# Kernel optimization log

Measured on AMD Instinct MI355X. Metric: run time of the kernel, lower is better.

## Reference

```python
import jax, jax.numpy as jnp
import numpy as np

N = 16384      # num_nodes
E = 524288     # num_edges (avg degree 32)
B = 32         # batch_size
D = 64         # input_dim
OUT = 64       # output_dim
K = 2          # max_diffusion_step
M = 2 * K + 1  # num_matrices = len(supports)*K + 1


def setup_inputs() -> dict:
    key = jax.random.key(0)
    k1, k2, k3, k4, k5 = jax.random.split(key, 5)
    inputs = jax.random.normal(k1, (B, N, D), dtype=jnp.float32)
    rows = jax.random.randint(k2, (E,), 0, N)
    cols = jax.random.randint(k3, (E,), 0, N)
    adj_vals = jax.random.uniform(k4, (E,), dtype=jnp.float32)
    # xavier_normal_ init for weights [D*M, OUT]
    std = (2.0 / (D * M + OUT)) ** 0.5
    weights = jax.random.normal(k5, (D * M, OUT), dtype=jnp.float32) * std
    biases = jnp.zeros((1, OUT), dtype=jnp.float32)  # bias_start = 0.0
    return dict(inputs=inputs, adj_vals=adj_vals, rows=rows, cols=cols,
                weights=weights, biases=biases)


def _spmm(vals, src, dst, x):
    # y[dst] += vals * x[src]; x: [N, F]  (sparse matrix-vector over edge list)
    return jax.ops.segment_sum(vals[:, None] * x[src], dst, num_segments=N)


def reference(inputs, adj_vals, rows, cols, weights, biases):
    b, n, d = inputs.shape
    # calculate_random_walk_matrix(A) = D_row^{-1} A ; support1 = its transpose
    # calculate_random_walk_matrix(A^T) = D_col^{-1} A^T ; support2 = its transpose
    drow = jax.ops.segment_sum(adj_vals, rows, num_segments=N)
    dcol = jax.ops.segment_sum(adj_vals, cols, num_segments=N)
    inv_drow = jnp.where(drow > 0, 1.0 / drow, 0.0)
    inv_dcol = jnp.where(dcol > 0, 1.0 / dcol, 0.0)
    vals1 = adj_vals * inv_drow[rows]  # support1 @ x: gather src=rows, scatter dst=cols
    vals2 = adj_vals * inv_dcol[cols]  # support2 @ x: gather src=cols, scatter dst=rows
    supports = [(vals1, rows, cols), (vals2, cols, rows)]

    # x0 layout: permute(1,2,0) -> [N, D, B] -> [N, D*B]
    x0 = jnp.transpose(inputs, (1, 2, 0)).reshape(n, d * b)
    xs = [x0]
    for vals, src, dst in supports:
        x1 = _spmm(vals, src, dst, x0)
        xs.append(x1)
        for _ in range(2, K + 1):
            x2 = 2.0 * _spmm(vals, src, dst, x1) - x0
            xs.append(x2)
            x1, x0 = x2, x1  # NOTE: x0 deliberately NOT reset between supports (matches torch src)
    x = jnp.stack(xs, axis=0).reshape(M, n, d, b)       # [M, N, D, B]
    x = jnp.transpose(x, (3, 1, 2, 0)).reshape(b * n, d * M)  # [B*N, D*M]
    out = x @ weights + biases
    return out.reshape(b, n, OUT)
```

## Files before the change

### kernel.cpp

```cpp
#include <hip/hip_runtime.h>
#include <stdint.h>

#define NN 16384
#define EE 524288
#define BB 32
#define DD 64
#define OO 64
#define MM 5
#define KK 320
#define KP 328

typedef __attribute__((ext_vector_type(8))) short short8;
typedef __attribute__((ext_vector_type(4))) float floatx4;

__device__ __forceinline__ float bf2f(unsigned short u) {
    return __uint_as_float(((unsigned int)u) << 16);
}
__device__ __forceinline__ unsigned short f2bf(float f) {
    unsigned int u = __float_as_uint(f);
    u += 0x7fffu + ((u >> 16) & 1u);
    return (unsigned short)(u >> 16);
}
__device__ __forceinline__ unsigned int pack2(float a, float b) {
    return (unsigned int)f2bf(a) | ((unsigned int)f2bf(b) << 16);
}

__global__ __launch_bounds__(256) void hist_kernel(
    const float* __restrict__ adj, const int* __restrict__ rows,
    const int* __restrict__ cols,
    float* __restrict__ drow, float* __restrict__ dcol,
    int* __restrict__ cnt_row, int* __restrict__ cnt_col)
{
    int e = blockIdx.x * 256 + threadIdx.x;
    if (e < EE) {
        float a = adj[e];
        int r = rows[e], c = cols[e];
        atomicAdd(&drow[r], a);
        atomicAdd(&dcol[c], a);
        atomicAdd(&cnt_row[r], 1);
        atomicAdd(&cnt_col[c], 1);
    }
}

__global__ __launch_bounds__(1024) void scan_kernel(
    const int* __restrict__ cnt_col, const int* __restrict__ cnt_row,
    int* __restrict__ off_col, int* __restrict__ off_row,
    int* __restrict__ cur_col, int* __restrict__ cur_row)
{
    const int* cnt = (blockIdx.x == 0) ? cnt_col : cnt_row;
    int* off = (blockIdx.x == 0) ? off_col : off_row;
    int* cur = (blockIdx.x == 0) ? cur_col : cur_row;

    __shared__ int part[1024];
    int t = threadIdx.x;
    int base = t * 16;
    int local[16];
    int s = 0;
#pragma unroll
    for (int i = 0; i < 16; i++) { local[i] = cnt[base + i]; s += local[i]; }
    part[t] = s;
    __syncthreads();
    for (int d = 1; d < 1024; d <<= 1) {
        int v = (t >= d) ? part[t - d] : 0;
        __syncthreads();
        part[t] += v;
        __syncthreads();
    }
    int run = (t == 0) ? 0 : part[t - 1];
#pragma unroll
    for (int i = 0; i < 16; i++) {
        off[base + i] = run;
        cur[base + i] = run;
        run += local[i];
    }
    if (t == 1023) off[NN] = run;
}

__global__ __launch_bounds__(256) void scatter_kernel(
    const float* __restrict__ adj, const int* __restrict__ rows,
    const int* __restrict__ cols,
    const float* __restrict__ drow, const float* __restrict__ dcol,
    int* __restrict__ cur_col, int* __restrict__ cur_row,
    int2* __restrict__ edge1, int2* __restrict__ edge2)
{
    int e = blockIdx.x * 256 + threadIdx.x;
    if (e < EE) {
        float a = adj[e];
        int r = rows[e], c = cols[e];
        float dr = drow[r];
        float idr = (dr > 0.f) ? (1.f / dr) : 0.f;
        float dc = dcol[c];
        float idc = (dc > 0.f) ? (1.f / dc) : 0.f;
        int p1 = atomicAdd(&cur_col[c], 1);
        edge1[p1] = make_int2(r, __float_as_int(a * idr));
        int p2 = atomicAdd(&cur_row[r], 1);
        edge2[p2] = make_int2(c, __float_as_int(a * idc));
    }
}

__global__ __launch_bounds__(256) void cast_kernel(
    const float* __restrict__ inp, unsigned short* __restrict__ x0)
{
    size_t i = ((size_t)blockIdx.x * 256 + threadIdx.x) * 8;
    float4 a = *(const float4*)(inp + i);
    float4 b = *(const float4*)(inp + i + 4);
    uint4 o;
    o.x = pack2(a.x, a.y);
    o.y = pack2(a.z, a.w);
    o.z = pack2(b.x, b.y);
    o.w = pack2(b.z, b.w);
    *(uint4*)(x0 + i) = o;
}

__global__ __launch_bounds__(256) void wprep_kernel(
    const float* __restrict__ W, unsigned short* __restrict__ Wt)
{
    int i = blockIdx.x * 256 + threadIdx.x;
    if (i < OO * KK) {
        int o = i / KK;
        int kp = i - o * KK;
        int m = kp >> 6;
        int d = kp & 63;
        Wt[i] = f2bf(W[(d * MM + m) * OO + o]);
    }
}

__global__ __launch_bounds__(256) void spmm_kernel(
    const unsigned short* __restrict__ xin,
    const unsigned short* __restrict__ z,
    unsigned short* __restrict__ xout,
    const int* __restrict__ off, const int2* __restrict__ edges,
    float alpha, float beta, int has_z)
{
    unsigned int l = blockIdx.x;
    int xcd  = l & 7;
    unsigned int s = l >> 3;
    int bhi  = s >> 9;
    int ntile = s & 511;
    int b = bhi * 8 + xcd;

    int t = threadIdx.x;
    int n = ntile * 32 + (t >> 3);
    unsigned int dgb = (unsigned int)(t & 7) * 16u;
    int e0 = off[n], e1 = off[n + 1];
    const char* xbB = (const char*)(xin + (size_t)b * NN * DD);

    float acc[8];
#pragma unroll
    for (int j = 0; j < 8; j++) acc[j] = 0.f;

#define FMA8(V, W)                                                        \
    do {                                                                  \
        acc[0] = fmaf((W), __uint_as_float((V).x << 16), acc[0]);         \
        acc[1] = fmaf((W), __uint_as_float((V).x & 0xffff0000u), acc[1]); \
        acc[2] = fmaf((W), __uint_as_float((V).y << 16), acc[2]);         \
        acc[3] = fmaf((W), __uint_as_float((V).y & 0xffff0000u), acc[3]); \
        acc[4] = fmaf((W), __uint_as_float((V).z << 16), acc[4]);         \
        acc[5] = fmaf((W), __uint_as_float((V).z & 0xffff0000u), acc[5]); \
        acc[6] = fmaf((W), __uint_as_float((V).w << 16), acc[6]);         \
        acc[7] = fmaf((W), __uint_as_float((V).w & 0xffff0000u), acc[7]); \
    } while (0)

    int ecnt = e1 - e0;
    int nb4 = ecnt >> 2;

    int2 ed0, ed1, ed2, ed3;
    if (nb4 > 0) {
        ed0 = edges[e0];
        ed1 = edges[e0 + 1];
        ed2 = edges[e0 + 2];
        ed3 = edges[e0 + 3];
    }
    for (int it = 0; it < nb4; ++it) {
        uint4 v0 = *(const uint4*)(xbB + (((unsigned int)ed0.x) << 7) + dgb);
        uint4 v1 = *(const uint4*)(xbB + (((unsigned int)ed1.x) << 7) + dgb);
        uint4 v2 = *(const uint4*)(xbB + (((unsigned int)ed2.x) << 7) + dgb);
        uint4 v3 = *(const uint4*)(xbB + (((unsigned int)ed3.x) << 7) + dgb);
        float w0 = __int_as_float(ed0.y);
        float w1 = __int_as_float(ed1.y);
        float w2 = __int_as_float(ed2.y);
        float w3 = __int_as_float(ed3.y);

        int2 nd0, nd1, nd2, nd3;
        int enext = e0 + (it + 1) * 4;
        if (it + 1 < nb4) {
            nd0 = edges[enext];
            nd1 = edges[enext + 1];
            nd2 = edges[enext + 2];
            nd3 = edges[enext + 3];
        }

        FMA8(v0, w0);
        FMA8(v1, w1);
        FMA8(v2, w2);
        FMA8(v3, w3);

        ed0 = nd0; ed1 = nd1; ed2 = nd2; ed3 = nd3;
    }
    for (int e = e0 + nb4 * 4; e < e1; ++e) {
        int2 ed = edges[e];
        float wv = __int_as_float(ed.y);
        uint4 v = *(const uint4*)(xbB + (((unsigned int)ed.x) << 7) + dgb);
        FMA8(v, wv);
    }
#undef FMA8

    size_t fo = ((size_t)b * NN + n) * DD + (dgb >> 1);
    if (has_z) {
        uint4 zv = *(const uint4*)(z + fo);
        float zf[8];
        zf[0] = __uint_as_float(zv.x << 16);
        zf[1] = __uint_as_float(zv.x & 0xffff0000u);
        zf[2] = __uint_as_float(zv.y << 16);
        zf[3] = __uint_as_float(zv.y & 0xffff0000u);
        zf[4] = __uint_as_float(zv.z << 16);
        zf[5] = __uint_as_float(zv.z & 0xffff0000u);
        zf[6] = __uint_as_float(zv.w << 16);
        zf[7] = __uint_as_float(zv.w & 0xffff0000u);
#pragma unroll
        for (int j = 0; j < 8; j++) acc[j] = alpha * acc[j] + beta * zf[j];
    }

    uint4 o;
    o.x = pack2(acc[0], acc[1]);
    o.y = pack2(acc[2], acc[3]);
    o.z = pack2(acc[4], acc[5]);
    o.w = pack2(acc[6], acc[7]);
    *(uint4*)(xout + fo) = o;
}

__global__ __launch_bounds__(256) void final_mfma(
    const unsigned short* __restrict__ X0, const unsigned short* __restrict__ X1,
    const unsigned short* __restrict__ X2, const unsigned short* __restrict__ X3,
    const unsigned short* __restrict__ X4,
    const unsigned short* __restrict__ Wt, const float* __restrict__ bias,
    float* __restrict__ out)
{
    __shared__ __align__(16) unsigned short A_lds[64 * KP];
    int blk = blockIdx.x;
    int b = blk >> 8;
    int n0 = (blk & 255) * 64;
    int t = threadIdx.x;
    const unsigned short* Xs[MM] = {X0, X1, X2, X3, X4};

#pragma unroll
    for (int i = 0; i < 10; i++) {
        int idx = t + i * 256;
        int dgv = (idx & 7) * 8;
        int row = (idx >> 3) & 63;
        int m = idx >> 9;
        uint4 v = *(const uint4*)(Xs[m] + ((size_t)b * NN + n0 + row) * DD + dgv);
        *(uint4*)&A_lds[row * KP + m * 64 + dgv] = v;
    }
    __syncthreads();

    int wave = t >> 6;
    int lane = t & 63;
    int col = lane & 15;
    int quad = lane >> 4;

    floatx4 acc[4];
#pragma unroll
    for (int ct = 0; ct < 4; ct++) acc[ct] = (floatx4){0.f, 0.f, 0.f, 0.f};

    const unsigned short* abase = &A_lds[(wave * 16 + col) * KP + quad * 8];
#pragma unroll
    for (int kt = 0; kt < 10; kt++) {
        short8 a = *(const short8*)(abase + kt * 32);
#pragma unroll
        for (int ct = 0; ct < 4; ct++) {
            short8 bf = *(const short8*)(Wt + (size_t)(ct * 16 + col) * KK + kt * 32 + quad * 8);
            acc[ct] = __builtin_amdgcn_mfma_f32_16x16x32_bf16(a, bf, acc[ct], 0, 0, 0);
        }
    }

    size_t rbase = (size_t)b * NN + n0 + wave * 16 + quad * 4;
#pragma unroll
    for (int ct = 0; ct < 4; ct++) {
        int o = ct * 16 + col;
        float bv = bias[o];
#pragma unroll
        for (int r = 0; r < 4; r++) {
            out[(rbase + r) * OO + o] = acc[ct][r] + bv;
        }
    }
}

extern "C" void kernel_launch(void* const* d_in, const int* in_sizes, int n_in,
                              void* d_out, int out_size, void* d_ws, size_t ws_size,
                              hipStream_t stream)
{
    (void)in_sizes; (void)n_in; (void)out_size; (void)ws_size;
    const float* inputs  = (const float*)d_in[0];
    const float* adj     = (const float*)d_in[1];
    const int*   rows    = (const int*)d_in[2];
    const int*   cols    = (const int*)d_in[3];
    const float* weights = (const float*)d_in[4];
    const float* bias    = (const float*)d_in[5];
    float* out = (float*)d_out;

    char* ws = (char*)d_ws;
    size_t off = 0;
    auto alloc = [&](size_t bytes) -> char* {
        char* p = ws + off;
        off = (off + bytes + 255) & ~(size_t)255;
        return p;
    };
    float* drow    = (float*)alloc(NN * 4);
    float* dcol    = (float*)alloc(NN * 4);
    int* cnt_col   = (int*)alloc(NN * 4);
    int* cnt_row   = (int*)alloc(NN * 4);
    int* off_col   = (int*)alloc((NN + 1) * 4);
    int* off_row   = (int*)alloc((NN + 1) * 4);
    int* cur_col   = (int*)alloc(NN * 4);
    int* cur_row   = (int*)alloc(NN * 4);
    int2* edge1    = (int2*)alloc((size_t)EE * 8);
    int2* edge2    = (int2*)alloc((size_t)EE * 8);
    unsigned short* Wt = (unsigned short*)alloc((size_t)OO * KK * 2);
    unsigned short* X[MM];
    for (int m = 0; m < MM; m++) X[m] = (unsigned short*)alloc((size_t)NN * BB * DD * 2);

    hipMemsetAsync(drow, 0, (size_t)NN * 4 * 4, stream);

    hist_kernel<<<EE / 256, 256, 0, stream>>>(adj, rows, cols, drow, dcol,
                                              cnt_row, cnt_col);
    scan_kernel<<<2, 1024, 0, stream>>>(cnt_col, cnt_row, off_col, off_row,
                                        cur_col, cur_row);
    scatter_kernel<<<EE / 256, 256, 0, stream>>>(adj, rows, cols, drow, dcol,
                                                 cur_col, cur_row, edge1, edge2);
    cast_kernel<<<(BB * NN * DD) / (256 * 8), 256, 0, stream>>>(inputs, X[0]);
    wprep_kernel<<<(OO * KK + 255) / 256, 256, 0, stream>>>(weights, Wt);

    const int SPMM_GRID = 512 * BB;

    spmm_kernel<<<SPMM_GRID, 256, 0, stream>>>(X[0], nullptr, X[1], off_col,
                                               edge1, 1.f, 0.f, 0);
    spmm_kernel<<<SPMM_GRID, 256, 0, stream>>>(X[1], X[0], X[2], off_col,
                                               edge1, 2.f, -1.f, 1);
    spmm_kernel<<<SPMM_GRID, 256, 0, stream>>>(X[1], nullptr, X[3], off_row,
                                               edge2, 1.f, 0.f, 0);
    spmm_kernel<<<SPMM_GRID, 256, 0, stream>>>(X[3], X[1], X[4], off_row,
                                               edge2, 2.f, -1.f, 1);

    final_mfma<<<BB * (NN / 64), 256, 0, stream>>>(X[0], X[1], X[2], X[3], X[4],
                                                   Wt, bias, out);
}
```

Baseline: 1.108 ms.

## Drop LDS staging in final GEMM and enlarge per-wave row tile to 64

The final dense projection kernel no longer stages the activation tile in shared memory. Each wave now loads its A fragments straight from global memory and computes a 64-row by 64-column output tile with 16 accumulators, so every weight fragment load is reused across four row tiles. Blocks cover 256 rows instead of 64, giving four times fewer blocks, and launch bounds request four blocks per SM. The aim is to remove the LDS round-trip and barrier and to cut redundant weight loads, at the cost of strided, less coalesced global loads for A and higher register pressure.

```diff
diff --git a/kernel.cpp b/kernel.cpp
--- a/kernel.cpp
+++ b/kernel.cpp
@@ -8,7 +8,6 @@
 #define OO 64
 #define MM 5
 #define KK 320
-#define KP 328
 
 typedef __attribute__((ext_vector_type(8))) short short8;
 typedef __attribute__((ext_vector_type(4))) float floatx4;
@@ -229,59 +228,83 @@
     *(uint4*)(xout + fo) = o;
 }
 
-__global__ __launch_bounds__(256) void final_mfma(
+__global__ __launch_bounds__(256, 4) void final_mfma(
     const unsigned short* __restrict__ X0, const unsigned short* __restrict__ X1,
     const unsigned short* __restrict__ X2, const unsigned short* __restrict__ X3,
     const unsigned short* __restrict__ X4,
     const unsigned short* __restrict__ Wt, const float* __restrict__ bias,
     float* __restrict__ out)
 {
-    __shared__ __align__(16) unsigned short A_lds[64 * KP];
     int blk = blockIdx.x;
-    int b = blk >> 8;
-    int n0 = (blk & 255) * 64;
+    int b = blk >> 6;
+    int n0 = (blk & 63) * 256;
     int t = threadIdx.x;
-    const unsigned short* Xs[MM] = {X0, X1, X2, X3, X4};
-
-#pragma unroll
-    for (int i = 0; i < 10; i++) {
-        int idx = t + i * 256;
-        int dgv = (idx & 7) * 8;
-        int row = (idx >> 3) & 63;
-        int m = idx >> 9;
-        uint4 v = *(const uint4*)(Xs[m] + ((size_t)b * NN + n0 + row) * DD + dgv);
-        *(uint4*)&A_lds[row * KP + m * 64 + dgv] = v;
-    }
-    __syncthreads();
-
     int wave = t >> 6;
     int lane = t & 63;
     int col = lane & 15;
     int quad = lane >> 4;
 
-    floatx4 acc[4];
-#pragma unroll
-    for (int ct = 0; ct < 4; ct++) acc[ct] = (floatx4){0.f, 0.f, 0.f, 0.f};
-
-    const unsigned short* abase = &A_lds[(wave * 16 + col) * KP + quad * 8];
-#pragma unroll
-    for (int kt = 0; kt < 10; kt++) {
-        short8 a = *(const short8*)(abase + kt * 32);
-#pragma unroll
-        for (int ct = 0; ct < 4; ct++) {
-            short8 bf = *(const short8*)(Wt + (size_t)(ct * 16 + col) * KK + kt * 32 + quad * 8);
-            acc[ct] = __builtin_amdgcn_mfma_f32_16x16x32_bf16(a, bf, acc[ct], 0, 0, 0);
-        }
-    }
-
-    size_t rbase = (size_t)b * NN + n0 + wave * 16 + quad * 4;
+    size_t rowbase = (size_t)b * NN + n0 + wave * 64;
+
+    floatx4 acc[4][4];
+#pragma unroll
+    for (int ct = 0; ct < 4; ct++)
+#pragma unroll
+        for (int rt = 0; rt < 4; rt++) acc[ct][rt] = (floatx4){0.f, 0.f, 0.f, 0.f};
+
+#define KSTEP(XP, m, h)                                                          \
+    {                                                                            \
+        const unsigned short* xa = (XP) + rowbase * DD + (h) * 32 + quad * 8;    \
+        short8 a0 = *(const short8*)(xa + (0 * 16 + col) * DD);                  \
+        short8 a1 = *(const short8*)(xa + (1 * 16 + col) * DD);                  \
+        short8 a2 = *(const short8*)(xa + (2 * 16 + col) * DD);                  \
+        short8 a3 = *(const short8*)(xa + (3 * 16 + col) * DD);                  \
+        const unsigned short* wb = Wt + ((m) * 2 + (h)) * 32 + quad * 8;         \
+        short8 b0 = *(const short8*)(wb + (0 * 16 + col) * KK);                  \
+        short8 b1 = *(const short8*)(wb + (1 * 16 + col) * KK);                  \
+        short8 b2 = *(const short8*)(wb + (2 * 16 + col) * KK);                  \
+        short8 b3 = *(const short8*)(wb + (3 * 16 + col) * KK);                  \
+        acc[0][0] = __builtin_amdgcn_mfma_f32_16x16x32_bf16(a0, b0, acc[0][0], 0, 0, 0); \
+        acc[0][1] = __builtin_amdgcn_mfma_f32_16x16x32_bf16(a1, b0, acc[0][1], 0, 0, 0); \
+        acc[0][2] = __builtin_amdgcn_mfma_f32_16x16x32_bf16(a2, b0, acc[0][2], 0, 0, 0); \
+        acc[0][3] = __builtin_amdgcn_mfma_f32_16x16x32_bf16(a3, b0, acc[0][3], 0, 0, 0); \
+        acc[1][0] = __builtin_amdgcn_mfma_f32_16x16x32_bf16(a0, b1, acc[1][0], 0, 0, 0); \
+        acc[1][1] = __builtin_amdgcn_mfma_f32_16x16x32_bf16(a1, b1, acc[1][1], 0, 0, 0); \
+        acc[1][2] = __builtin_amdgcn_mfma_f32_16x16x32_bf16(a2, b1, acc[1][2], 0, 0, 0); \
+        acc[1][3] = __builtin_amdgcn_mfma_f32_16x16x32_bf16(a3, b1, acc[1][3], 0, 0, 0); \
+        acc[2][0] = __builtin_amdgcn_mfma_f32_16x16x32_bf16(a0, b2, acc[2][0], 0, 0, 0); \
+        acc[2][1] = __builtin_amdgcn_mfma_f32_16x16x32_bf16(a1, b2, acc[2][1], 0, 0, 0); \
+        acc[2][2] = __builtin_amdgcn_mfma_f32_16x16x32_bf16(a2, b2, acc[2][2], 0, 0, 0); \
+        acc[2][3] = __builtin_amdgcn_mfma_f32_16x16x32_bf16(a3, b2, acc[2][3], 0, 0, 0); \
+        acc[3][0] = __builtin_amdgcn_mfma_f32_16x16x32_bf16(a0, b3, acc[3][0], 0, 0, 0); \
+        acc[3][1] = __builtin_amdgcn_mfma_f32_16x16x32_bf16(a1, b3, acc[3][1], 0, 0, 0); \
+        acc[3][2] = __builtin_amdgcn_mfma_f32_16x16x32_bf16(a2, b3, acc[3][2], 0, 0, 0); \
+        acc[3][3] = __builtin_amdgcn_mfma_f32_16x16x32_bf16(a3, b3, acc[3][3], 0, 0, 0); \
+    }
+
+    KSTEP(X0, 0, 0)
+    KSTEP(X0, 0, 1)
+    KSTEP(X1, 1, 0)
+    KSTEP(X1, 1, 1)
+    KSTEP(X2, 2, 0)
+    KSTEP(X2, 2, 1)
+    KSTEP(X3, 3, 0)
+    KSTEP(X3, 3, 1)
+    KSTEP(X4, 4, 0)
+    KSTEP(X4, 4, 1)
+#undef KSTEP
+
 #pragma unroll
     for (int ct = 0; ct < 4; ct++) {
         int o = ct * 16 + col;
         float bv = bias[o];
 #pragma unroll
-        for (int r = 0; r < 4; r++) {
-            out[(rbase + r) * OO + o] = acc[ct][r] + bv;
+        for (int rt = 0; rt < 4; rt++) {
+            size_t rb = rowbase + rt * 16 + quad * 4;
+#pragma unroll
+            for (int r = 0; r < 4; r++) {
+                out[(rb + r) * OO + o] = acc[ct][rt][r] + bv;
+            }
         }
     }
 }
@@ -342,6 +365,6 @@
     spmm_kernel<<<SPMM_GRID, 256, 0, stream>>>(X[3], X[1], X[4], off_row,
                                                edge2, 2.f, -1.f, 1);
 
-    final_mfma<<<BB * (NN / 64), 256, 0, stream>>>(X[0], X[1], X[2], X[3], X[4],
-                                                   Wt, bias, out);
-}
+    final_mfma<<<BB * (NN / 256), 256, 0, stream>>>(X[0], X[1], X[2], X[3], X[4],
+                                                    Wt, bias, out);
+}
```

Measured after the change: 1.043 ms. -5.9%, faster.
